# Optimization experiments

Hardware: AMD Instinct MI355X
Metric: run time of the kernel (lower is better)

The kernel has to match this reference:

```python
import jax, jax.numpy as jnp
import numpy as np

B, S, H, HEADS = 4, 2048, 512, 8
DK = H // HEADS
LN_EPS = 1e-5
NEG_INF = -1e30


def setup_inputs() -> dict:
    key = jax.random.key(0)
    k = jax.random.split(key, 6)
    x = jax.random.normal(k[0], (B, S, H), dtype=jnp.float32)
    mask = jax.random.randint(k[1], (B, S), 0, 2, dtype=jnp.int32)
    # per-head Q/K/V projection weights stacked: [heads, H, dk]
    Wq = jax.random.normal(k[2], (HEADS, H, DK), dtype=jnp.float32) * 0.05
    Wk = jax.random.normal(k[3], (HEADS, H, DK), dtype=jnp.float32) * 0.05
    Wv = jax.random.normal(k[4], (HEADS, H, DK), dtype=jnp.float32) * 0.05
    # output projection: [heads*dk, H] (y = h @ Wo)
    Wo = jax.random.normal(k[5], (HEADS * DK, H), dtype=jnp.float32) * 0.05
    gamma = jnp.ones((H,), dtype=jnp.float32)
    beta = jnp.zeros((H,), dtype=jnp.float32)
    return {"x": x, "mask": mask, "Wq": Wq, "Wk": Wk, "Wv": Wv,
            "Wo": Wo, "gamma": gamma, "beta": beta}


def reference(x, mask, Wq, Wk, Wv, Wo, gamma, beta):
    # LayerNorm over hidden dim
    mu = jnp.mean(x, axis=-1, keepdims=True)
    var = jnp.mean(jnp.square(x - mu), axis=-1, keepdims=True)
    xn = (x - mu) * jax.lax.rsqrt(var + LN_EPS) * gamma + beta  # [B,S,H]

    mf = mask.astype(jnp.float32)  # [B,S]

    # batched per-head projections (original loops over heads)
    q = jnp.einsum('bsh,nhd->bnsd', xn, Wq)  # [B,heads,S,dk]
    kk = jnp.einsum('bsh,nhd->bnsd', xn, Wk)
    v = jnp.einsum('bsh,nhd->bnsd', xn, Wv)

    scores = jnp.einsum('bnqd,bnkd->bnqk', q, kk) / np.sqrt(DK).astype(np.float32)
    m = mf[:, None, None, :]  # [B,1,1,S] broadcast over query dim
    logits = m * scores + (1.0 - m) * NEG_INF
    probs = jax.nn.softmax(logits, axis=-1)
    attn = jnp.einsum('bnqk,bnkd->bnqd', probs, v)  # [B,heads,S,dk]

    h = attn.transpose(0, 2, 1, 3).reshape(x.shape[0], x.shape[1], HEADS * DK)
    out = h @ Wo + xn          # residual adds post-norm x (as in original)
    out = out * mf[:, :, None]  # zero out masked positions
    return out
```

## Files before the change

kernel.cpp:

```cpp
#include <hip/hip_runtime.h>
#include <hip/hip_bf16.h>
#include <math.h>

#define B_ 4
#define S_ 2048
#define H_ 512
#define HEADS_ 8
#define DK_ 64
#define NROWS_ (B_*S_)
#define LN_EPS_ 1e-5f
#define NEG_INF_ -1e30f
#define QSCALE_ (0.125f * 1.44269504088896f)

typedef short s8v __attribute__((ext_vector_type(8)));
typedef short s4v __attribute__((ext_vector_type(4)));
typedef float f4v __attribute__((ext_vector_type(4)));

typedef __attribute__((address_space(1))) unsigned int gu32_t;
typedef __attribute__((address_space(3))) unsigned int lu32_t;

__device__ __forceinline__ unsigned short f2bf(float f) {
    unsigned int u = __float_as_uint(f);
    u += 0x7FFFu + ((u >> 16) & 1u);
    return (unsigned short)(u >> 16);
}

__device__ __forceinline__ s4v pk4bf(float a, float b, float c, float d) {
    union { __hip_bfloat162 h[2]; s4v v; } u;
    u.h[0] = __float22bfloat162_rn(float2{a, b});
    u.h[1] = __float22bfloat162_rn(float2{c, d});
    return u.v;
}

__global__ __launch_bounds__(256) void wt_kernel(
        const float* __restrict__ Wq, const float* __restrict__ Wk,
        const float* __restrict__ Wv, const float* __restrict__ Wo,
        unsigned short* __restrict__ Wt) {
    __shared__ float tile[32][33];
    int z = blockIdx.z;
    int k0 = blockIdx.y * 32, c0 = blockIdx.x * 32;
    const float* src;
    int ld, drow;
    float scale = 1.f;
    if (z < 24) {
        if (blockIdx.x >= 2) return;
        int zw = z >> 3, head = z & 7;
        const float* W = (zw == 0) ? Wq : (zw == 1) ? Wk : Wv;
        if (zw == 0) scale = QSCALE_;
        src = W + (size_t)head * H_ * DK_;
        ld = DK_;
        drow = zw * 512 + head * 64;
    } else {
        src = Wo; ld = H_; drow = 1536;
    }
    int tx = threadIdx.x & 31, ty = threadIdx.x >> 5;
    #pragma unroll
    for (int i = 0; i < 4; i++)
        tile[ty * 4 + i][tx] = src[(size_t)(k0 + ty * 4 + i) * ld + c0 + tx];
    __syncthreads();
    #pragma unroll
    for (int i = 0; i < 4; i++) {
        int cc = ty * 4 + i;
        Wt[(size_t)(drow + c0 + cc) * 512 + k0 + tx] = f2bf(tile[tx][cc] * scale);
    }
}

__global__ __launch_bounds__(256) void ln_kernel(
        const float* __restrict__ x, const float* __restrict__ gamma,
        const float* __restrict__ beta, const int* __restrict__ mask,
        float* __restrict__ xn, unsigned short* __restrict__ xnb,
        float* __restrict__ mb) {
    int row  = blockIdx.x * 4 + (threadIdx.x >> 6);
    int lane = threadIdx.x & 63;
    const float4* xr = (const float4*)(x + (size_t)row * H_ + lane * 8);
    float4 a = xr[0], d = xr[1];
    float s  = (a.x + a.y) + (a.z + a.w) + (d.x + d.y) + (d.z + d.w);
    float ss = (a.x*a.x + a.y*a.y) + (a.z*a.z + a.w*a.w)
             + (d.x*d.x + d.y*d.y) + (d.z*d.z + d.w*d.w);
    #pragma unroll
    for (int i = 1; i < 64; i <<= 1) {
        s  += __shfl_xor(s, i, 64);
        ss += __shfl_xor(ss, i, 64);
    }
    float mu  = s * (1.f / 512.f);
    float var = ss * (1.f / 512.f) - mu * mu;
    float rstd = rsqrtf(var + LN_EPS_);
    if (lane == 0) mb[row] = mask[row] ? 0.f : NEG_INF_;
    const float4* gp = (const float4*)(gamma + lane * 8);
    const float4* bp = (const float4*)(beta + lane * 8);
    float4 g0 = gp[0], g1 = gp[1], b0 = bp[0], b1 = bp[1];
    float4 y0, y1;
    y0.x = (a.x - mu) * rstd * g0.x + b0.x;
    y0.y = (a.y - mu) * rstd * g0.y + b0.y;
    y0.z = (a.z - mu) * rstd * g0.z + b0.z;
    y0.w = (a.w - mu) * rstd * g0.w + b0.w;
    y1.x = (d.x - mu) * rstd * g1.x + b1.x;
    y1.y = (d.y - mu) * rstd * g1.y + b1.y;
    y1.z = (d.z - mu) * rstd * g1.z + b1.z;
    y1.w = (d.w - mu) * rstd * g1.w + b1.w;
    float4* xo = (float4*)(xn + (size_t)row * H_ + lane * 8);
    xo[0] = y0; xo[1] = y1;
    union { s4v h[2]; s8v v; } pk;
    pk.h[0] = pk4bf(y0.x, y0.y, y0.z, y0.w);
    pk.h[1] = pk4bf(y1.x, y1.y, y1.z, y1.w);
    *(s8v*)(xnb + (size_t)row * H_ + lane * 8) = pk.v;
}

#define BK_ 32
__device__ __forceinline__ void gemm_tile(
        const unsigned short* __restrict__ A,
        const unsigned short* __restrict__ Bt,
        int r0, int j0, f4v acc[4][4]) {
    __shared__ unsigned short As[128 * BK_];
    __shared__ unsigned short Bs[128 * BK_];
    int t = threadIdx.x;
    int wv = t >> 6, L = t & 63, c = L & 15, g = L >> 4;
    int m_base = (wv & 1) * 64, n_base = (wv >> 1) * 64;
    #pragma unroll
    for (int i = 0; i < 4; i++)
        #pragma unroll
        for (int j = 0; j < 4; j++) acc[i][j] = (f4v){0.f, 0.f, 0.f, 0.f};
    for (int k0 = 0; k0 < 512; k0 += BK_) {
        __syncthreads();
        #pragma unroll
        for (int i = 0; i < 2; i++) {
            int u = wv * 128 + i * 64 + L;
            int row = u >> 2, k8 = u & 3;
            __builtin_amdgcn_global_load_lds(
                (const gu32_t*)(A + (size_t)(r0 + row) * 512 + k0 + k8 * 8),
                (lu32_t*)(As + (size_t)(wv * 128 + i * 64) * 8), 16, 0, 0);
            __builtin_amdgcn_global_load_lds(
                (const gu32_t*)(Bt + (size_t)(j0 + row) * 512 + k0 + k8 * 8),
                (lu32_t*)(Bs + (size_t)(wv * 128 + i * 64) * 8), 16, 0, 0);
        }
        __asm__ volatile("s_waitcnt vmcnt(0)" ::: "memory");
        __syncthreads();
        s8v a[4], b[4];
        #pragma unroll
        for (int i = 0; i < 4; i++)
            a[i] = *(const s8v*)(As + (size_t)(m_base + i * 16 + c) * BK_ + g * 8);
        #pragma unroll
        for (int j = 0; j < 4; j++)
            b[j] = *(const s8v*)(Bs + (size_t)(n_base + j * 16 + c) * BK_ + g * 8);
        #pragma unroll
        for (int i = 0; i < 4; i++)
            #pragma unroll
            for (int j = 0; j < 4; j++)
                acc[i][j] = __builtin_amdgcn_mfma_f32_16x16x32_bf16(
                    a[i], b[j], acc[i][j], 0, 0, 0);
    }
}

__global__ __launch_bounds__(256) void qkv_gemm(
        const unsigned short* __restrict__ xnb,
        const unsigned short* __restrict__ Wt,
        unsigned short* __restrict__ Qb, unsigned short* __restrict__ Kf,
        unsigned short* __restrict__ Vf) {
    f4v acc[4][4];
    int t = threadIdx.x;
    int wv = t >> 6, L = t & 63, c = L & 15, g = L >> 4;
    int rb = wv & 1, cb = wv >> 1;
    if (blockIdx.x < 8) {
        int m0 = blockIdx.x * 128, n0 = blockIdx.y * 128;
        gemm_tile(Wt, xnb, m0, n0, acc);
        int R0 = m0 + rb * 64;
        int C0 = n0 + cb * 64;
        int hd = (R0 >> 6) & 7;
        int b  = C0 >> 11, srow0 = C0 & 2047;
        size_t bhbase = (size_t)(b * HEADS_ + hd) * S_ * DK_;
        if (R0 < 512) {
            #pragma unroll
            for (int msub = 0; msub < 4; msub++) {
                int dk4 = msub * 16 + g * 4;
                #pragma unroll
                for (int nsub = 0; nsub < 4; nsub++) {
                    int tok = srow0 + nsub * 16 + c;
                    s4v v = pk4bf(acc[msub][nsub][0], acc[msub][nsub][1],
                                  acc[msub][nsub][2], acc[msub][nsub][3]);
                    *(s4v*)(Qb + bhbase + (size_t)tok * DK_ + dk4) = v;
                }
            }
        } else {
            unsigned short* dst = Kf + bhbase + (size_t)(srow0 >> 6) * 4096;
            #pragma unroll
            for (int msub = 0; msub < 4; msub++) {
                int gx = (msub & 1) * 2 + (g >> 1);
                int slotbase = (g & 1) * 4 + (msub >> 1) * 8;
                #pragma unroll
                for (int nsub = 0; nsub < 4; nsub++) {
                    s4v v = pk4bf(acc[msub][nsub][0], acc[msub][nsub][1],
                                  acc[msub][nsub][2], acc[msub][nsub][3]);
                    *(s4v*)(dst + nsub * 1024 + (gx * 16 + c) * 16 + slotbase) = v;
                }
            }
        }
    } else {
        int r0 = blockIdx.y * 128, j0 = 1024 + (blockIdx.x - 8) * 128;
        gemm_tile(xnb, Wt, r0, j0, acc);
        int R0 = r0 + rb * 64;
        int C0 = j0 + cb * 64;
        int hd = (C0 >> 6) & 7;
        int b = R0 >> 11, srow0 = R0 & 2047;
        unsigned short* dst = Vf + (size_t)(b * HEADS_ + hd) * S_ * DK_
                              + (size_t)(srow0 >> 6) * 4096;
        #pragma unroll
        for (int msub = 0; msub < 4; msub++)
            #pragma unroll
            for (int nsub = 0; nsub < 4; nsub++) {
                s4v v = pk4bf(acc[msub][nsub][0], acc[msub][nsub][1],
                              acc[msub][nsub][2], acc[msub][nsub][3]);
                *(s4v*)(dst + nsub * 1024 + (g * 16 + c) * 16 + msub * 4) = v;
            }
    }
}

__global__ __launch_bounds__(256, 3) void attn_kernel(
        const unsigned short* __restrict__ Qb,
        const unsigned short* __restrict__ Kf,
        const unsigned short* __restrict__ Vf,
        const float* __restrict__ mb,
        unsigned short* __restrict__ hb) {
    __shared__ float red[2][64][2][17];

    int wv   = threadIdx.x >> 6;
    int qsub = wv & 1;
    int kp   = wv >> 1;
    int L  = threadIdx.x & 63;
    int c  = L & 15;
    int g  = L >> 4;
    int bh = blockIdx.y;
    int b  = bh >> 3, n = bh & 7;
    int q0 = blockIdx.x * 64 + qsub * 32;

    const unsigned short* Qbase = Qb + (size_t)bh * S_ * DK_;
    const unsigned short* Kp = Kf + (size_t)bh * S_ * DK_ + (size_t)kp * 16 * 4096 + L * 16;
    const unsigned short* Vp = Vf + (size_t)bh * S_ * DK_ + (size_t)kp * 16 * 4096 + L * 16;
    const float* mbrow = mb + b * S_ + kp * 1024;

    s8v qfA0 = *(const s8v*)(Qbase + (size_t)(q0 + c) * DK_ + g * 8);
    s8v qfA1 = *(const s8v*)(Qbase + (size_t)(q0 + c) * DK_ + 32 + g * 8);
    s8v qfB0 = *(const s8v*)(Qbase + (size_t)(q0 + 16 + c) * DK_ + g * 8);
    s8v qfB1 = *(const s8v*)(Qbase + (size_t)(q0 + 16 + c) * DK_ + 32 + g * 8);

    f4v accA[4], accB[4];
    #pragma unroll
    for (int i = 0; i < 4; i++) {
        accA[i] = (f4v){0.f, 0.f, 0.f, 0.f};
        accB[i] = (f4v){0.f, 0.f, 0.f, 0.f};
    }
    float lacA[4] = {0.f, 0.f, 0.f, 0.f};
    float lacB[4] = {0.f, 0.f, 0.f, 0.f};

    for (int kb = 0; kb < 16; kb++) {
        const unsigned short* Kn = Kp + (size_t)kb * 4096;
        const unsigned short* Vn = Vp + (size_t)kb * 4096;
        #pragma unroll
        for (int h = 0; h < 2; h++) {
            s8v k0lo = *(const s8v*)(Kn + (h * 2 + 0) * 1024);
            s8v k0hi = *(const s8v*)(Kn + (h * 2 + 0) * 1024 + 8);
            s8v k1lo = *(const s8v*)(Kn + (h * 2 + 1) * 1024);
            s8v k1hi = *(const s8v*)(Kn + (h * 2 + 1) * 1024 + 8);
            float4 mb0 = *(const float4*)(mbrow + kb * 64 + h * 32 + g * 4);
            float4 mb1 = *(const float4*)(mbrow + kb * 64 + h * 32 + 16 + g * 4);
            s8v vv[4];
            #pragma unroll
            for (int ds = 0; ds < 4; ds++)
                vv[ds] = *(const s8v*)(Vn + ds * 1024 + h * 8);
            f4v bias0 = (f4v){mb0.x, mb0.y, mb0.z, mb0.w};
            f4v bias1 = (f4v){mb1.x, mb1.y, mb1.z, mb1.w};
            f4v sA0 = bias0, sA1 = bias1, sB0 = bias0, sB1 = bias1;
            sA0 = __builtin_amdgcn_mfma_f32_16x16x32_bf16(k0lo, qfA0, sA0, 0, 0, 0);
            sA0 = __builtin_amdgcn_mfma_f32_16x16x32_bf16(k0hi, qfA1, sA0, 0, 0, 0);
            sA1 = __builtin_amdgcn_mfma_f32_16x16x32_bf16(k1lo, qfA0, sA1, 0, 0, 0);
            sA1 = __builtin_amdgcn_mfma_f32_16x16x32_bf16(k1hi, qfA1, sA1, 0, 0, 0);
            sB0 = __builtin_amdgcn_mfma_f32_16x16x32_bf16(k0lo, qfB0, sB0, 0, 0, 0);
            sB0 = __builtin_amdgcn_mfma_f32_16x16x32_bf16(k0hi, qfB1, sB0, 0, 0, 0);
            sB1 = __builtin_amdgcn_mfma_f32_16x16x32_bf16(k1lo, qfB0, sB1, 0, 0, 0);
            sB1 = __builtin_amdgcn_mfma_f32_16x16x32_bf16(k1hi, qfB1, sB1, 0, 0, 0);
            float pA0[4], pA1[4], pB0[4], pB1[4];
            #pragma unroll
            for (int r = 0; r < 4; r++) {
                pA0[r] = __builtin_amdgcn_exp2f(sA0[r]);
                pA1[r] = __builtin_amdgcn_exp2f(sA1[r]);
                pB0[r] = __builtin_amdgcn_exp2f(sB0[r]);
                pB1[r] = __builtin_amdgcn_exp2f(sB1[r]);
                lacA[r] += pA0[r] + pA1[r];
                lacB[r] += pB0[r] + pB1[r];
            }
            s4v pfA0 = pk4bf(pA0[0], pA0[1], pA0[2], pA0[3]);
            s4v pfA1 = pk4bf(pA1[0], pA1[1], pA1[2], pA1[3]);
            s4v pfB0 = pk4bf(pB0[0], pB0[1], pB0[2], pB0[3]);
            s4v pfB1 = pk4bf(pB1[0], pB1[1], pB1[2], pB1[3]);
            #pragma unroll
            for (int ds = 0; ds < 4; ds++) {
                s4v v0 = __builtin_shufflevector(vv[ds], vv[ds], 0, 1, 2, 3);
                s4v v1 = __builtin_shufflevector(vv[ds], vv[ds], 4, 5, 6, 7);
                accA[ds] = __builtin_amdgcn_mfma_f32_16x16x16bf16_1k(v0, pfA0, accA[ds], 0, 0, 0);
                accA[ds] = __builtin_amdgcn_mfma_f32_16x16x16bf16_1k(v1, pfA1, accA[ds], 0, 0, 0);
                accB[ds] = __builtin_amdgcn_mfma_f32_16x16x16bf16_1k(v0, pfB0, accB[ds], 0, 0, 0);
                accB[ds] = __builtin_amdgcn_mfma_f32_16x16x16bf16_1k(v1, pfB1, accB[ds], 0, 0, 0);
            }
        }
    }

    float lA = (lacA[0] + lacA[1]) + (lacA[2] + lacA[3]);
    float lB = (lacB[0] + lacB[1]) + (lacB[2] + lacB[3]);
    lA += __shfl_xor(lA, 16, 64);
    lA += __shfl_xor(lA, 32, 64);
    lB += __shfl_xor(lB, 16, 64);
    lB += __shfl_xor(lB, 32, 64);

    if (kp == 1) {
        #pragma unroll
        for (int d = 0; d < 4; d++) {
            #pragma unroll
            for (int r = 0; r < 4; r++) {
                red[qsub][L][0][d * 4 + r] = accA[d][r];
                red[qsub][L][1][d * 4 + r] = accB[d][r];
            }
        }
        red[qsub][L][0][16] = lA;
        red[qsub][L][1][16] = lB;
    }
    __syncthreads();
    if (kp == 0) {
        const float* srcA = &red[qsub][L][0][0];
        const float* srcB = &red[qsub][L][1][0];
        float invA = 1.f / (lA + srcA[16]);
        float invB = 1.f / (lB + srcB[16]);
        unsigned short* hpA = hb + (size_t)(b * S_ + q0 + c) * H_ + n * DK_ + g * 4;
        unsigned short* hpB = hpA + (size_t)16 * H_;
        #pragma unroll
        for (int ds = 0; ds < 4; ds++) {
            s4v oA = pk4bf((accA[ds][0] + srcA[ds * 4 + 0]) * invA,
                           (accA[ds][1] + srcA[ds * 4 + 1]) * invA,
                           (accA[ds][2] + srcA[ds * 4 + 2]) * invA,
                           (accA[ds][3] + srcA[ds * 4 + 3]) * invA);
            *(s4v*)(hpA + ds * 16) = oA;
            s4v oB = pk4bf((accB[ds][0] + srcB[ds * 4 + 0]) * invB,
                           (accB[ds][1] + srcB[ds * 4 + 1]) * invB,
                           (accB[ds][2] + srcB[ds * 4 + 2]) * invB,
                           (accB[ds][3] + srcB[ds * 4 + 3]) * invB);
            *(s4v*)(hpB + ds * 16) = oB;
        }
    }
}

__global__ __launch_bounds__(256) void out_gemm(
        const unsigned short* __restrict__ hb,
        const unsigned short* __restrict__ Wot,
        const float* __restrict__ xn, const int* __restrict__ mask,
        float* __restrict__ out) {
    f4v acc[4][4];
    int r0 = blockIdx.y * 128, j0 = blockIdx.x * 128;
    gemm_tile(hb, Wot, r0, j0, acc);
    int t = threadIdx.x;
    int wv = t >> 6, L = t & 63, c = L & 15, g = L >> 4;
    int mrow = r0 + (wv & 1) * 64 + g * 4;
    int ncol = j0 + (wv >> 1) * 64 + c;
    #pragma unroll
    for (int msub = 0; msub < 4; msub++) {
        #pragma unroll
        for (int rr = 0; rr < 4; rr++) {
            int row = mrow + msub * 16 + rr;
            float mf = (float)mask[row];
            #pragma unroll
            for (int nsub = 0; nsub < 4; nsub++) {
                int col = ncol + nsub * 16;
                size_t o = (size_t)row * H_ + col;
                out[o] = (acc[msub][nsub][rr] + xn[o]) * mf;
            }
        }
    }
}

extern "C" void kernel_launch(void* const* d_in, const int* in_sizes, int n_in,
                              void* d_out, int out_size, void* d_ws, size_t ws_size,
                              hipStream_t stream) {
    const float* x     = (const float*)d_in[0];
    const int*   mask  = (const int*)d_in[1];
    const float* Wq    = (const float*)d_in[2];
    const float* Wk    = (const float*)d_in[3];
    const float* Wv    = (const float*)d_in[4];
    const float* Wo    = (const float*)d_in[5];
    const float* gamma = (const float*)d_in[6];
    const float* beta  = (const float*)d_in[7];
    float* out = (float*)d_out;

    size_t nelem = (size_t)NROWS_ * H_;
    char* ws = (char*)d_ws;
    float*          xn  = (float*)ws;          ws += nelem * 4;
    unsigned short* xnb = (unsigned short*)ws; ws += nelem * 2;
    unsigned short* hb  = (unsigned short*)ws; ws += nelem * 2;
    unsigned short* Qb  = (unsigned short*)ws; ws += nelem * 2;
    unsigned short* Kf  = (unsigned short*)ws; ws += nelem * 2;
    unsigned short* Vf  = (unsigned short*)ws; ws += nelem * 2;
    unsigned short* Wt  = (unsigned short*)ws; ws += (size_t)2048 * 512 * 2;
    float*          mbp = (float*)ws;

    wt_kernel<<<dim3(16, 16, 25), 256, 0, stream>>>(Wq, Wk, Wv, Wo, Wt);
    ln_kernel<<<NROWS_ / 4, 256, 0, stream>>>(x, gamma, beta, mask, xn, xnb, mbp);
    qkv_gemm<<<dim3(12, 64), 256, 0, stream>>>(xnb, Wt, Qb, Kf, Vf);
    attn_kernel<<<dim3(S_ / 64, B_ * HEADS_), 256, 0, stream>>>(
        Qb, Kf, Vf, mbp, hb);
    out_gemm<<<dim3(4, 64), 256, 0, stream>>>(
        hb, Wt + (size_t)1536 * 512, xn, mask, out);
}
```

Measured before the change: 185.5 us.

## Fuse LN and weight prep, drop fp32 xn, deepen GEMM K-step, raise attn occupancy

Merges the weight transpose/convert kernel and the LayerNorm kernel into one launch that also skips the idle blocks the old 3D grid wasted. It stops writing the fp32 normalized activations and has the output GEMM read the bf16 copy for the residual, which cuts memory traffic but lowers residual precision. The shared GEMM tile now loads 64 K-elements per barrier instead of 32, halving the sync count. The attention kernel's launch bound moves from 3 to 4 blocks per CU, which may force register spills.

```diff
diff --git a/kernel.cpp b/kernel.cpp
--- a/kernel.cpp
+++ b/kernel.cpp
@@ -25,6 +25,10 @@
     return (unsigned short)(u >> 16);
 }
 
+__device__ __forceinline__ float bf2f(unsigned short u) {
+    return __uint_as_float((unsigned int)u << 16);
+}
+
 __device__ __forceinline__ s4v pk4bf(float a, float b, float c, float d) {
     union { __hip_bfloat162 h[2]; s4v v; } u;
     u.h[0] = __float22bfloat162_rn(float2{a, b});
@@ -32,87 +36,88 @@
     return u.v;
 }
 
-__global__ __launch_bounds__(256) void wt_kernel(
+__global__ __launch_bounds__(256) void prep_kernel(
+        const float* __restrict__ x, const float* __restrict__ gamma,
+        const float* __restrict__ beta, const int* __restrict__ mask,
         const float* __restrict__ Wq, const float* __restrict__ Wk,
         const float* __restrict__ Wv, const float* __restrict__ Wo,
+        unsigned short* __restrict__ xnb, float* __restrict__ mb,
         unsigned short* __restrict__ Wt) {
-    __shared__ float tile[32][33];
-    int z = blockIdx.z;
-    int k0 = blockIdx.y * 32, c0 = blockIdx.x * 32;
-    const float* src;
-    int ld, drow;
-    float scale = 1.f;
-    if (z < 24) {
-        if (blockIdx.x >= 2) return;
-        int zw = z >> 3, head = z & 7;
-        const float* W = (zw == 0) ? Wq : (zw == 1) ? Wk : Wv;
-        if (zw == 0) scale = QSCALE_;
-        src = W + (size_t)head * H_ * DK_;
-        ld = DK_;
-        drow = zw * 512 + head * 64;
+    int bx = blockIdx.x;
+    if (bx < 2048) {
+        int row  = bx * 4 + (threadIdx.x >> 6);
+        int lane = threadIdx.x & 63;
+        const float4* xr = (const float4*)(x + (size_t)row * H_ + lane * 8);
+        float4 a = xr[0], d = xr[1];
+        float s  = (a.x + a.y) + (a.z + a.w) + (d.x + d.y) + (d.z + d.w);
+        float ss = (a.x*a.x + a.y*a.y) + (a.z*a.z + a.w*a.w)
+                 + (d.x*d.x + d.y*d.y) + (d.z*d.z + d.w*d.w);
+        #pragma unroll
+        for (int i = 1; i < 64; i <<= 1) {
+            s  += __shfl_xor(s, i, 64);
+            ss += __shfl_xor(ss, i, 64);
+        }
+        float mu  = s * (1.f / 512.f);
+        float var = ss * (1.f / 512.f) - mu * mu;
+        float rstd = rsqrtf(var + LN_EPS_);
+        if (lane == 0) mb[row] = mask[row] ? 0.f : NEG_INF_;
+        const float4* gp = (const float4*)(gamma + lane * 8);
+        const float4* bp = (const float4*)(beta + lane * 8);
+        float4 g0 = gp[0], g1 = gp[1], b0 = bp[0], b1 = bp[1];
+        float4 y0, y1;
+        y0.x = (a.x - mu) * rstd * g0.x + b0.x;
+        y0.y = (a.y - mu) * rstd * g0.y + b0.y;
+        y0.z = (a.z - mu) * rstd * g0.z + b0.z;
+        y0.w = (a.w - mu) * rstd * g0.w + b0.w;
+        y1.x = (d.x - mu) * rstd * g1.x + b1.x;
+        y1.y = (d.y - mu) * rstd * g1.y + b1.y;
+        y1.z = (d.z - mu) * rstd * g1.z + b1.z;
+        y1.w = (d.w - mu) * rstd * g1.w + b1.w;
+        union { s4v h[2]; s8v v; } pk;
+        pk.h[0] = pk4bf(y0.x, y0.y, y0.z, y0.w);
+        pk.h[1] = pk4bf(y1.x, y1.y, y1.z, y1.w);
+        *(s8v*)(xnb + (size_t)row * H_ + lane * 8) = pk.v;
     } else {
-        src = Wo; ld = H_; drow = 1536;
-    }
-    int tx = threadIdx.x & 31, ty = threadIdx.x >> 5;
-    #pragma unroll
-    for (int i = 0; i < 4; i++)
-        tile[ty * 4 + i][tx] = src[(size_t)(k0 + ty * 4 + i) * ld + c0 + tx];
-    __syncthreads();
-    #pragma unroll
-    for (int i = 0; i < 4; i++) {
-        int cc = ty * 4 + i;
-        Wt[(size_t)(drow + c0 + cc) * 512 + k0 + tx] = f2bf(tile[tx][cc] * scale);
-    }
-}
-
-__global__ __launch_bounds__(256) void ln_kernel(
-        const float* __restrict__ x, const float* __restrict__ gamma,
-        const float* __restrict__ beta, const int* __restrict__ mask,
-        float* __restrict__ xn, unsigned short* __restrict__ xnb,
-        float* __restrict__ mb) {
-    int row  = blockIdx.x * 4 + (threadIdx.x >> 6);
-    int lane = threadIdx.x & 63;
-    const float4* xr = (const float4*)(x + (size_t)row * H_ + lane * 8);
-    float4 a = xr[0], d = xr[1];
-    float s  = (a.x + a.y) + (a.z + a.w) + (d.x + d.y) + (d.z + d.w);
-    float ss = (a.x*a.x + a.y*a.y) + (a.z*a.z + a.w*a.w)
-             + (d.x*d.x + d.y*d.y) + (d.z*d.z + d.w*d.w);
-    #pragma unroll
-    for (int i = 1; i < 64; i <<= 1) {
-        s  += __shfl_xor(s, i, 64);
-        ss += __shfl_xor(ss, i, 64);
-    }
-    float mu  = s * (1.f / 512.f);
-    float var = ss * (1.f / 512.f) - mu * mu;
-    float rstd = rsqrtf(var + LN_EPS_);
-    if (lane == 0) mb[row] = mask[row] ? 0.f : NEG_INF_;
-    const float4* gp = (const float4*)(gamma + lane * 8);
-    const float4* bp = (const float4*)(beta + lane * 8);
-    float4 g0 = gp[0], g1 = gp[1], b0 = bp[0], b1 = bp[1];
-    float4 y0, y1;
-    y0.x = (a.x - mu) * rstd * g0.x + b0.x;
-    y0.y = (a.y - mu) * rstd * g0.y + b0.y;
-    y0.z = (a.z - mu) * rstd * g0.z + b0.z;
-    y0.w = (a.w - mu) * rstd * g0.w + b0.w;
-    y1.x = (d.x - mu) * rstd * g1.x + b1.x;
-    y1.y = (d.y - mu) * rstd * g1.y + b1.y;
-    y1.z = (d.z - mu) * rstd * g1.z + b1.z;
-    y1.w = (d.w - mu) * rstd * g1.w + b1.w;
-    float4* xo = (float4*)(xn + (size_t)row * H_ + lane * 8);
-    xo[0] = y0; xo[1] = y1;
-    union { s4v h[2]; s8v v; } pk;
-    pk.h[0] = pk4bf(y0.x, y0.y, y0.z, y0.w);
-    pk.h[1] = pk4bf(y1.x, y1.y, y1.z, y1.w);
-    *(s8v*)(xnb + (size_t)row * H_ + lane * 8) = pk.v;
-}
-
-#define BK_ 32
+        __shared__ float tile[32][33];
+        int wid = bx - 2048;
+        const float* src;
+        int ld, drow, k0, c0;
+        float scale = 1.f;
+        if (wid < 768) {
+            int z = wid >> 5, rem = wid & 31;
+            int cx = rem & 1, ky = rem >> 1;
+            k0 = ky * 32; c0 = cx * 32;
+            int zw = z >> 3, head = z & 7;
+            const float* W = (zw == 0) ? Wq : (zw == 1) ? Wk : Wv;
+            if (zw == 0) scale = QSCALE_;
+            src = W + (size_t)head * H_ * DK_;
+            ld = DK_;
+            drow = zw * 512 + head * 64;
+        } else {
+            int rem = wid - 768;
+            int cx = rem & 15, ky = rem >> 4;
+            k0 = ky * 32; c0 = cx * 32;
+            src = Wo; ld = H_; drow = 1536;
+        }
+        int tx = threadIdx.x & 31, ty = threadIdx.x >> 5;
+        #pragma unroll
+        for (int i = 0; i < 4; i++)
+            tile[ty * 4 + i][tx] = src[(size_t)(k0 + ty * 4 + i) * ld + c0 + tx];
+        __syncthreads();
+        #pragma unroll
+        for (int i = 0; i < 4; i++) {
+            int cc = ty * 4 + i;
+            Wt[(size_t)(drow + c0 + cc) * 512 + k0 + tx] = f2bf(tile[tx][cc] * scale);
+        }
+    }
+}
+
 __device__ __forceinline__ void gemm_tile(
         const unsigned short* __restrict__ A,
         const unsigned short* __restrict__ Bt,
         int r0, int j0, f4v acc[4][4]) {
-    __shared__ unsigned short As[128 * BK_];
-    __shared__ unsigned short Bs[128 * BK_];
+    __shared__ unsigned short As[2 * 128 * 32];
+    __shared__ unsigned short Bs[2 * 128 * 32];
     int t = threadIdx.x;
     int wv = t >> 6, L = t & 63, c = L & 15, g = L >> 4;
     int m_base = (wv & 1) * 64, n_base = (wv >> 1) * 64;
@@ -120,34 +125,40 @@
     for (int i = 0; i < 4; i++)
         #pragma unroll
         for (int j = 0; j < 4; j++) acc[i][j] = (f4v){0.f, 0.f, 0.f, 0.f};
-    for (int k0 = 0; k0 < 512; k0 += BK_) {
+    for (int k0 = 0; k0 < 512; k0 += 64) {
         __syncthreads();
         #pragma unroll
-        for (int i = 0; i < 2; i++) {
-            int u = wv * 128 + i * 64 + L;
-            int row = u >> 2, k8 = u & 3;
-            __builtin_amdgcn_global_load_lds(
-                (const gu32_t*)(A + (size_t)(r0 + row) * 512 + k0 + k8 * 8),
-                (lu32_t*)(As + (size_t)(wv * 128 + i * 64) * 8), 16, 0, 0);
-            __builtin_amdgcn_global_load_lds(
-                (const gu32_t*)(Bt + (size_t)(j0 + row) * 512 + k0 + k8 * 8),
-                (lu32_t*)(Bs + (size_t)(wv * 128 + i * 64) * 8), 16, 0, 0);
+        for (int half = 0; half < 2; half++) {
+            #pragma unroll
+            for (int i = 0; i < 2; i++) {
+                int u = wv * 128 + i * 64 + L;
+                int row = u >> 2, k16 = u & 3;
+                __builtin_amdgcn_global_load_lds(
+                    (const gu32_t*)(A + (size_t)(r0 + row) * 512 + k0 + half * 32 + k16 * 8),
+                    (lu32_t*)(As + half * 4096 + (size_t)(wv * 128 + i * 64) * 8), 16, 0, 0);
+                __builtin_amdgcn_global_load_lds(
+                    (const gu32_t*)(Bt + (size_t)(j0 + row) * 512 + k0 + half * 32 + k16 * 8),
+                    (lu32_t*)(Bs + half * 4096 + (size_t)(wv * 128 + i * 64) * 8), 16, 0, 0);
+            }
         }
         __asm__ volatile("s_waitcnt vmcnt(0)" ::: "memory");
         __syncthreads();
-        s8v a[4], b[4];
-        #pragma unroll
-        for (int i = 0; i < 4; i++)
-            a[i] = *(const s8v*)(As + (size_t)(m_base + i * 16 + c) * BK_ + g * 8);
-        #pragma unroll
-        for (int j = 0; j < 4; j++)
-            b[j] = *(const s8v*)(Bs + (size_t)(n_base + j * 16 + c) * BK_ + g * 8);
-        #pragma unroll
-        for (int i = 0; i < 4; i++)
+        #pragma unroll
+        for (int half = 0; half < 2; half++) {
+            s8v a[4], b[4];
+            #pragma unroll
+            for (int i = 0; i < 4; i++)
+                a[i] = *(const s8v*)(As + half * 4096 + (size_t)(m_base + i * 16 + c) * 32 + g * 8);
             #pragma unroll
             for (int j = 0; j < 4; j++)
-                acc[i][j] = __builtin_amdgcn_mfma_f32_16x16x32_bf16(
-                    a[i], b[j], acc[i][j], 0, 0, 0);
+                b[j] = *(const s8v*)(Bs + half * 4096 + (size_t)(n_base + j * 16 + c) * 32 + g * 8);
+            #pragma unroll
+            for (int i = 0; i < 4; i++)
+                #pragma unroll
+                for (int j = 0; j < 4; j++)
+                    acc[i][j] = __builtin_amdgcn_mfma_f32_16x16x32_bf16(
+                        a[i], b[j], acc[i][j], 0, 0, 0);
+        }
     }
 }
 
@@ -214,7 +225,7 @@
     }
 }
 
-__global__ __launch_bounds__(256, 3) void attn_kernel(
+__global__ __launch_bounds__(256, 4) void attn_kernel(
         const unsigned short* __restrict__ Qb,
         const unsigned short* __restrict__ Kf,
         const unsigned short* __restrict__ Vf,
@@ -349,7 +360,7 @@
 __global__ __launch_bounds__(256) void out_gemm(
         const unsigned short* __restrict__ hb,
         const unsigned short* __restrict__ Wot,
-        const float* __restrict__ xn, const int* __restrict__ mask,
+        const unsigned short* __restrict__ xnb, const int* __restrict__ mask,
         float* __restrict__ out) {
     f4v acc[4][4];
     int r0 = blockIdx.y * 128, j0 = blockIdx.x * 128;
@@ -368,7 +379,7 @@
             for (int nsub = 0; nsub < 4; nsub++) {
                 int col = ncol + nsub * 16;
                 size_t o = (size_t)row * H_ + col;
-                out[o] = (acc[msub][nsub][rr] + xn[o]) * mf;
+                out[o] = (acc[msub][nsub][rr] + bf2f(xnb[o])) * mf;
             }
         }
     }
@@ -389,7 +400,6 @@
 
     size_t nelem = (size_t)NROWS_ * H_;
     char* ws = (char*)d_ws;
-    float*          xn  = (float*)ws;          ws += nelem * 4;
     unsigned short* xnb = (unsigned short*)ws; ws += nelem * 2;
     unsigned short* hb  = (unsigned short*)ws; ws += nelem * 2;
     unsigned short* Qb  = (unsigned short*)ws; ws += nelem * 2;
@@ -398,11 +408,11 @@
     unsigned short* Wt  = (unsigned short*)ws; ws += (size_t)2048 * 512 * 2;
     float*          mbp = (float*)ws;
 
-    wt_kernel<<<dim3(16, 16, 25), 256, 0, stream>>>(Wq, Wk, Wv, Wo, Wt);
-    ln_kernel<<<NROWS_ / 4, 256, 0, stream>>>(x, gamma, beta, mask, xn, xnb, mbp);
+    prep_kernel<<<3072, 256, 0, stream>>>(
+        x, gamma, beta, mask, Wq, Wk, Wv, Wo, xnb, mbp, Wt);
     qkv_gemm<<<dim3(12, 64), 256, 0, stream>>>(xnb, Wt, Qb, Kf, Vf);
     attn_kernel<<<dim3(S_ / 64, B_ * HEADS_), 256, 0, stream>>>(
         Qb, Kf, Vf, mbp, hb);
     out_gemm<<<dim3(4, 64), 256, 0, stream>>>(
-        hb, Wt + (size_t)1536 * 512, xn, mask, out);
-}
+        hb, Wt + (size_t)1536 * 512, xnb, mask, out);
+}
```

Measured after the change: 192.3 us. +3.7%, slower.
